# Optimization experiments

Measured on AMD Instinct MI355X. Metric: run time of the kernel, lower is better.

## Reference

```python
import jax, jax.numpy as jnp
import numpy as np

DIM = 128
HEADS = 4
GN_GROUPS = 4
EPS = 1e-5


def setup_inputs() -> dict:
    key = jax.random.key(0)
    ks = jax.random.split(key, 6)
    B, C, H, W = 4, DIM, 64, 64
    x = jax.random.normal(ks[0], (B, C, H, W), dtype=jnp.float32)
    # 1x1 convs are channel matmuls: store as [out_ch, in_ch]
    w_qkv = jax.random.normal(ks[1], (3 * C, C), dtype=jnp.float32) * (C ** -0.5)
    w_out = jax.random.normal(ks[2], (C, C), dtype=jnp.float32) * (C ** -0.5)
    b_out = jax.random.normal(ks[3], (C,), dtype=jnp.float32) * 0.01
    gn_gamma = jnp.ones((C,), dtype=jnp.float32)
    gn_beta = jnp.zeros((C,), dtype=jnp.float32)
    return {"x": x, "w_qkv": w_qkv, "w_out": w_out, "b_out": b_out,
            "gn_gamma": gn_gamma, "gn_beta": gn_beta}


def _attention_block(x, w_qkv, w_out, b_out, gn_gamma, gn_beta):
    b, c, h, w = x.shape
    d = c // HEADS
    scale = d ** -0.5
    # 1x1 conv == per-pixel matmul over channels
    qkv = jnp.einsum('bchw,oc->bohw', x, w_qkv)  # [b, 3c, h, w]
    q, k, v = jnp.split(qkv, 3, axis=1)
    # 'b (h d) x y -> b h (x y) d'
    def to_heads(t):
        return t.reshape(b, HEADS, d, h * w).transpose(0, 1, 3, 2)  # [b, H, N, d]
    q, k, v = to_heads(q), to_heads(k), to_heads(v)
    dots = jnp.einsum('bhnd,bhmd->bhnm', q, k) * scale  # [b, H, N, N]
    attn = jax.nn.softmax(dots, axis=-1)
    out = jnp.einsum('bhnm,bhmd->bhnd', attn, v)  # [b, H, N, d]
    # 'b h (x y) d -> b (h d) x y'
    out = out.transpose(0, 1, 3, 2).reshape(b, c, h, w)
    # output 1x1 conv + bias
    out = jnp.einsum('bchw,oc->bohw', out, w_out) + b_out[None, :, None, None]
    # GroupNorm(4, c)
    g = out.reshape(b, GN_GROUPS, c // GN_GROUPS, h, w)
    mean = g.mean(axis=(2, 3, 4), keepdims=True)
    var = g.var(axis=(2, 3, 4), keepdims=True)
    g = (g - mean) * jax.lax.rsqrt(var + EPS)
    out = g.reshape(b, c, h, w) * gn_gamma[None, :, None, None] + gn_beta[None, :, None, None]
    return out + x


def reference(x, w_qkv, w_out, b_out, gn_gamma, gn_beta):
    return _attention_block(x, w_qkv, w_out, b_out, gn_gamma, gn_beta)
```

## Files before the change

### kernel.cpp

```cpp
#include <hip/hip_runtime.h>

#define DIM   128
#define NPIX  4096
#define DHEAD 32

using u16 = unsigned short;
typedef __attribute__((ext_vector_type(8))) short   short8;
typedef __attribute__((ext_vector_type(8))) u16     ushort8;
typedef __attribute__((ext_vector_type(4))) float   floatx4;
typedef __attribute__((ext_vector_type(2))) unsigned int uint2v;

__device__ __forceinline__ float bf2f(u16 u) {
  union { unsigned int i; float f; } v; v.i = ((unsigned int)u) << 16; return v.f;
}
__device__ __forceinline__ u16 f2bf(float f) {
  union { unsigned int i; float f; } v; v.f = f;
  unsigned int i = v.i;
  return (u16)((i + 0x7FFFu + ((i >> 16) & 1u)) >> 16);
}
__device__ __forceinline__ unsigned int pk2bf(float a, float b) {
  union { float f; unsigned int u; } ua, ub; ua.f = a; ub.f = b;
  return __builtin_amdgcn_perm(ub.u, ua.u, 0x07060302u);
}

template<bool F32> __device__ __forceinline__ float ld1(const void* p, size_t i) {
  if constexpr (F32) return ((const float*)p)[i];
  else               return bf2f(((const u16*)p)[i]);
}
template<bool F32> __device__ __forceinline__ float4 ld4(const void* p, size_t i) {
  if constexpr (F32) {
    return *(const float4*)((const float*)p + i);
  } else {
    const ushort4 u = *(const ushort4*)((const u16*)p + i);
    return make_float4(bf2f(u.x), bf2f(u.y), bf2f(u.z), bf2f(u.w));
  }
}
template<bool F32> __device__ __forceinline__ void st4(void* p, size_t i, float4 v) {
  if constexpr (F32) {
    *(float4*)((float*)p + i) = v;
  } else {
    ushort4 u; u.x = f2bf(v.x); u.y = f2bf(v.y); u.z = f2bf(v.z); u.w = f2bf(v.w);
    *(ushort4*)((u16*)p + i) = u;
  }
}

__global__ void k_detect(const u16* __restrict__ x, int* __restrict__ flag) {
  if (threadIdx.x == 0 && blockIdx.x == 0) {
    int big = 0;
    for (int i = 0; i < 128; ++i) {
      const float v = bf2f(x[i]);
      if (!(fabsf(v) < 1e4f)) big = 1;
    }
    *flag = big;
  }
}

template<bool F32>
__global__ __launch_bounds__(256) void k_qkv(const void* __restrict__ x,
                                             const void* __restrict__ wqkv,
                                             u16* __restrict__ Q,
                                             u16* __restrict__ K,
                                             u16* __restrict__ V,
                                             const int* __restrict__ flag) {
  if (*flag != (F32 ? 1 : 0)) return;
  const int b = blockIdx.z, og = blockIdx.y, pt = blockIdx.x;
  const int tl = threadIdx.x;
  __shared__ float Ws[8][DIM];
  for (int i = tl; i < 8 * DIM; i += 256)
    Ws[i >> 7][i & 127] = ld1<F32>(wqkv, (size_t)(og * 8 + (i >> 7)) * DIM + (i & 127));
  __syncthreads();
  const int p0 = pt * 1024 + tl * 4;
  float acc[8][4];
#pragma unroll
  for (int j = 0; j < 8; ++j) { acc[j][0] = acc[j][1] = acc[j][2] = acc[j][3] = 0.f; }
  const size_t xb = (size_t)b * DIM * NPIX + p0;
  for (int c = 0; c < DIM; ++c) {
    const float4 xv = ld4<F32>(x, xb + (size_t)c * NPIX);
#pragma unroll
    for (int j = 0; j < 8; ++j) {
      const float wv = Ws[j][c];
      acc[j][0] += wv * xv.x; acc[j][1] += wv * xv.y;
      acc[j][2] += wv * xv.z; acc[j][3] += wv * xv.w;
    }
  }
  const int o0 = og * 8;
  if (o0 < 2 * DIM) {
    u16* dst = (o0 < DIM) ? Q : K;
    const int c0 = o0 & 127;
    const int h = c0 >> 5, dd0 = c0 & 31;
    const int bh = b * 4 + h;
#pragma unroll
    for (int t = 0; t < 4; ++t) {
      ushort8 w8;
#pragma unroll
      for (int j = 0; j < 8; ++j) w8[j] = f2bf(acc[j][t]);
      *(ushort8*)(dst + ((size_t)bh * NPIX + p0 + t) * DHEAD + dd0) = w8;
    }
  } else {
#pragma unroll
    for (int j = 0; j < 8; ++j) {
      const int c = (o0 + j) & 127;
      ushort4 w4;
      w4.x = f2bf(acc[j][0]); w4.y = f2bf(acc[j][1]);
      w4.z = f2bf(acc[j][2]); w4.w = f2bf(acc[j][3]);
      *(ushort4*)(V + ((size_t)b * DIM + c) * NPIX + p0) = w4;
    }
  }
}

__global__ __launch_bounds__(256) void k_attn(const u16* __restrict__ Q,
                                              const u16* __restrict__ K,
                                              const u16* __restrict__ V,
                                              u16* __restrict__ O) {
  const int bh = blockIdx.y, qb = blockIdx.x;
  const int tid = threadIdx.x;
  const int wv = tid >> 6, lane = tid & 63;
  const int quad = lane >> 4, l15 = lane & 15;
  const int b = bh >> 2, h = bh & 3;

  __shared__ __align__(16) u16 Klds[64 * 40];
  __shared__ __align__(16) u16 Vlds[32 * 72];
  __shared__ __align__(16) u16 Plds[4 * 16 * 72];
  __shared__ __align__(16) u16 Olds[32 * 72];

  const float SCL = 0.17677669529663687f * 1.4426950408889634f;

  const int qtok = qb * 64 + wv * 16 + l15;
  const short8 qf = *(const short8*)(Q + ((size_t)bh * NPIX + qtok) * DHEAD + quad * 8);

  floatx4 o0 = {0.f, 0.f, 0.f, 0.f}, o1 = {0.f, 0.f, 0.f, 0.f};
  float l_part = 0.f;

  const int skey = tid >> 2, sqt = tid & 3;
  const int sdd = tid >> 3, soc = tid & 7;
  const u16* Kg = K + ((size_t)bh * NPIX + skey) * DHEAD + sqt * 8;
  const u16* Vg = V + ((size_t)(b * DIM + h * DHEAD + sdd)) * NPIX + soc * 8;

  ushort8 kpre = *(const ushort8*)Kg;
  ushort8 vpre = *(const ushort8*)Vg;

  u16* Pw = Plds + wv * 16 * 72;

  for (int ch = 0; ch < 64; ++ch) {
    *(ushort8*)(Klds + skey * 40 + sqt * 8) = kpre;
    *(ushort8*)(Vlds + sdd * 72 + soc * 8) = vpre;
    __syncthreads();
    if (ch + 1 < 64) {
      kpre = *(const ushort8*)(Kg + (size_t)(ch + 1) * 64 * DHEAD);
      vpre = *(const ushort8*)(Vg + (ch + 1) * 64);
    }
#pragma unroll
    for (int sub = 0; sub < 4; ++sub) {
      const short8 af = *(const short8*)(Klds + (sub * 16 + l15) * 40 + quad * 8);
      const floatx4 s = __builtin_amdgcn_mfma_f32_16x16x32_bf16(
          af, qf, (floatx4){0.f, 0.f, 0.f, 0.f}, 0, 0, 0);
      const float p0 = __builtin_amdgcn_exp2f(s[0] * SCL);
      const float p1 = __builtin_amdgcn_exp2f(s[1] * SCL);
      const float p2 = __builtin_amdgcn_exp2f(s[2] * SCL);
      const float p3 = __builtin_amdgcn_exp2f(s[3] * SCL);
      l_part += (p0 + p1) + (p2 + p3);
      uint2v pw;
      pw[0] = pk2bf(p0, p1);
      pw[1] = pk2bf(p2, p3);
      *(uint2v*)(Pw + l15 * 72 + sub * 16 + quad * 4) = pw;
    }
#pragma unroll
    for (int kc = 0; kc < 2; ++kc) {
      const short8 pa  = *(const short8*)(Pw + l15 * 72 + kc * 32 + quad * 8);
      const short8 vb0 = *(const short8*)(Vlds + l15 * 72 + kc * 32 + quad * 8);
      const short8 vb1 = *(const short8*)(Vlds + (16 + l15) * 72 + kc * 32 + quad * 8);
      o0 = __builtin_amdgcn_mfma_f32_16x16x32_bf16(pa, vb0, o0, 0, 0, 0);
      o1 = __builtin_amdgcn_mfma_f32_16x16x32_bf16(pa, vb1, o1, 0, 0, 0);
    }
    __syncthreads();
  }
  float l_run = l_part;
  l_run += __shfl_xor(l_run, 16);
  l_run += __shfl_xor(l_run, 32);
  float linv[4];
#pragma unroll
  for (int r = 0; r < 4; ++r)
    linv[r] = 1.f / __shfl(l_run, (lane & 48) | (quad * 4 + r));
  uint2v w0, w1;
  w0[0] = (unsigned)f2bf(o0[0] * linv[0]) | ((unsigned)f2bf(o0[1] * linv[1]) << 16);
  w0[1] = (unsigned)f2bf(o0[2] * linv[2]) | ((unsigned)f2bf(o0[3] * linv[3]) << 16);
  w1[0] = (unsigned)f2bf(o1[0] * linv[0]) | ((unsigned)f2bf(o1[1] * linv[1]) << 16);
  w1[1] = (unsigned)f2bf(o1[2] * linv[2]) | ((unsigned)f2bf(o1[3] * linv[3]) << 16);
  *(uint2v*)(Olds + l15 * 72 + wv * 16 + quad * 4) = w0;
  *(uint2v*)(Olds + (16 + l15) * 72 + wv * 16 + quad * 4) = w1;
  __syncthreads();
  const int d = tid >> 3, oc = tid & 7;
  const ushort8 ow = *(const ushort8*)(Olds + d * 72 + oc * 8);
  *(ushort8*)(O + ((size_t)(b * DIM + h * DHEAD + d)) * NPIX + qb * 64 + oc * 8) = ow;
}

template<bool F32>
__global__ __launch_bounds__(256) void k_proj(const u16* __restrict__ O,
                                              const void* __restrict__ wout,
                                              const void* __restrict__ bout,
                                              float* __restrict__ Y,
                                              float* __restrict__ Sred,
                                              const int* __restrict__ flag) {
  if (*flag != (F32 ? 1 : 0)) return;
  const int b = blockIdx.z, og = blockIdx.y, pt = blockIdx.x;
  const int tl = threadIdx.x;
  __shared__ float Ws[8][DIM];
  for (int i = tl; i < 8 * DIM; i += 256)
    Ws[i >> 7][i & 127] = ld1<F32>(wout, (size_t)(og * 8 + (i >> 7)) * DIM + (i & 127));
  __syncthreads();
  const int p0 = pt * 1024 + tl * 4;
  float acc[8][4];
#pragma unroll
  for (int j = 0; j < 8; ++j) { acc[j][0] = acc[j][1] = acc[j][2] = acc[j][3] = 0.f; }
  const u16* Ob = O + (size_t)b * DIM * NPIX + p0;
  for (int c = 0; c < DIM; ++c) {
    const ushort4 xv4 = *(const ushort4*)(Ob + (size_t)c * NPIX);
    const float x0 = bf2f(xv4.x), x1 = bf2f(xv4.y), x2 = bf2f(xv4.z), x3 = bf2f(xv4.w);
#pragma unroll
    for (int j = 0; j < 8; ++j) {
      const float wv = Ws[j][c];
      acc[j][0] += wv * x0; acc[j][1] += wv * x1;
      acc[j][2] += wv * x2; acc[j][3] += wv * x3;
    }
  }
  float s1 = 0.f, s2 = 0.f;
#pragma unroll
  for (int j = 0; j < 8; ++j) {
    const int o = og * 8 + j;
    const float bo = ld1<F32>(bout, o);
    float4 y4;
    y4.x = acc[j][0] + bo; y4.y = acc[j][1] + bo;
    y4.z = acc[j][2] + bo; y4.w = acc[j][3] + bo;
    *(float4*)(Y + ((size_t)b * DIM + o) * NPIX + p0) = y4;
    s1 += y4.x + y4.y + y4.z + y4.w;
    s2 += y4.x * y4.x + y4.y * y4.y + y4.z * y4.z + y4.w * y4.w;
  }
  __shared__ float red[2][256];
  red[0][tl] = s1; red[1][tl] = s2;
  __syncthreads();
  for (int off = 128; off >= 1; off >>= 1) {
    if (tl < off) { red[0][tl] += red[0][tl + off]; red[1][tl] += red[1][tl + off]; }
    __syncthreads();
  }
  if (tl == 0) {
    const int g = og >> 2;
    atomicAdd(&Sred[(b * 4 + g) * 2 + 0], red[0][0]);
    atomicAdd(&Sred[(b * 4 + g) * 2 + 1], red[1][0]);
  }
}

template<bool F32>
__global__ __launch_bounds__(256) void k_gn(const float* __restrict__ Y,
                                            const float* __restrict__ Sred,
                                            const void* __restrict__ x,
                                            const void* __restrict__ gamma,
                                            const void* __restrict__ beta,
                                            void* __restrict__ out,
                                            const int* __restrict__ flag) {
  if (*flag != (F32 ? 1 : 0)) return;
  const int idx = (blockIdx.x * 256 + threadIdx.x) * 4;
  const int b = idx >> 19;
  const int c = (idx >> 12) & 127;
  const int g = c >> 5;
  const float inv_n = 1.f / (32.f * 4096.f);
  const float s1 = Sred[(b * 4 + g) * 2 + 0];
  const float s2 = Sred[(b * 4 + g) * 2 + 1];
  const float mean = s1 * inv_n;
  const float var = s2 * inv_n - mean * mean;
  const float rs = rsqrtf(var + 1e-5f);
  const float ga = ld1<F32>(gamma, c) * rs;
  const float be = ld1<F32>(beta, c) - mean * ga;
  const float4 y4 = *(const float4*)(Y + idx);
  const float4 xv = ld4<F32>(x, idx);
  float4 r;
  r.x = y4.x * ga + be + xv.x;
  r.y = y4.y * ga + be + xv.y;
  r.z = y4.z * ga + be + xv.z;
  r.w = y4.w * ga + be + xv.w;
  st4<F32>(out, idx, r);
}

extern "C" void kernel_launch(void* const* d_in, const int* in_sizes, int n_in,
                              void* d_out, int out_size, void* d_ws, size_t ws_size,
                              hipStream_t stream) {
  const void* x     = d_in[0];
  const void* wqkv  = d_in[1];
  const void* wout  = d_in[2];
  const void* bout  = d_in[3];
  const void* gamma = d_in[4];
  const void* beta  = d_in[5];
  char* ws = (char*)d_ws;
  u16*   Q = (u16*)(ws + ((size_t)0  << 20));
  u16*   K = (u16*)(ws + ((size_t)8  << 20));
  u16*   V = (u16*)(ws + ((size_t)16 << 20));
  u16*   O = (u16*)(ws + ((size_t)24 << 20));
  float* Y = (float*)(ws + ((size_t)32 << 20));
  float* S = (float*)(ws + ((size_t)40 << 20));
  int*   F = (int*)(ws + ((size_t)40 << 20) + 128);

  hipMemsetAsync(S, 0, 160, stream);
  k_detect<<<1, 64, 0, stream>>>((const u16*)x, F);

  k_qkv<false><<<dim3(4, 48, 4), 256, 0, stream>>>(x, wqkv, Q, K, V, F);
  k_qkv<true> <<<dim3(4, 48, 4), 256, 0, stream>>>(x, wqkv, Q, K, V, F);
  k_attn<<<dim3(64, 16), 256, 0, stream>>>(Q, K, V, O);
  k_proj<false><<<dim3(4, 16, 4), 256, 0, stream>>>(O, wout, bout, Y, S, F);
  k_proj<true> <<<dim3(4, 16, 4), 256, 0, stream>>>(O, wout, bout, Y, S, F);
  k_gn<false><<<2048, 256, 0, stream>>>(Y, S, x, gamma, beta, d_out, F);
  k_gn<true> <<<2048, 256, 0, stream>>>(Y, S, x, gamma, beta, d_out, F);
}
```

Before: 221.3 us.

## Process 32 queries per wave and double-buffer K/V tiles in attention

Each attention block now covers 128 queries instead of 64, with each wave handling two 16-query tiles. Every K/V tile staged in shared memory is therefore reused across twice as many queries, halving global K/V traffic per query. The K/V shared buffers are also double-buffered, which removes one barrier per chunk. In exchange the grid halves to 512 blocks, which may underfill the GPU's 256 CUs, and register and LDS use per block rise.

New measurement: 214.2 us. 1.03x faster.

```diff
diff --git a/kernel.cpp b/kernel.cpp
--- a/kernel.cpp
+++ b/kernel.cpp
@@ -118,80 +118,111 @@
   const int quad = lane >> 4, l15 = lane & 15;
   const int b = bh >> 2, h = bh & 3;
 
-  __shared__ __align__(16) u16 Klds[64 * 40];
-  __shared__ __align__(16) u16 Vlds[32 * 72];
-  __shared__ __align__(16) u16 Plds[4 * 16 * 72];
-  __shared__ __align__(16) u16 Olds[32 * 72];
+  __shared__ __align__(16) u16 Klds[2][64 * 40];
+  __shared__ __align__(16) u16 Vlds[2][32 * 72];
+  __shared__ __align__(16) u16 Plds[4][32 * 72];
+  __shared__ __align__(16) u16 Olds[32 * 136];
 
   const float SCL = 0.17677669529663687f * 1.4426950408889634f;
 
-  const int qtok = qb * 64 + wv * 16 + l15;
-  const short8 qf = *(const short8*)(Q + ((size_t)bh * NPIX + qtok) * DHEAD + quad * 8);
-
-  floatx4 o0 = {0.f, 0.f, 0.f, 0.f}, o1 = {0.f, 0.f, 0.f, 0.f};
-  float l_part = 0.f;
+  const int qtok0 = qb * 128 + wv * 32 + l15;
+  const short8 qf0 = *(const short8*)(Q + ((size_t)bh * NPIX + qtok0) * DHEAD + quad * 8);
+  const short8 qf1 = *(const short8*)(Q + ((size_t)bh * NPIX + qtok0 + 16) * DHEAD + quad * 8);
+
+  floatx4 o00 = {0.f, 0.f, 0.f, 0.f}, o01 = {0.f, 0.f, 0.f, 0.f};
+  floatx4 o10 = {0.f, 0.f, 0.f, 0.f}, o11 = {0.f, 0.f, 0.f, 0.f};
+  float lp0 = 0.f, lp1 = 0.f;
 
   const int skey = tid >> 2, sqt = tid & 3;
   const int sdd = tid >> 3, soc = tid & 7;
   const u16* Kg = K + ((size_t)bh * NPIX + skey) * DHEAD + sqt * 8;
   const u16* Vg = V + ((size_t)(b * DIM + h * DHEAD + sdd)) * NPIX + soc * 8;
 
-  ushort8 kpre = *(const ushort8*)Kg;
-  ushort8 vpre = *(const ushort8*)Vg;
-
-  u16* Pw = Plds + wv * 16 * 72;
+  {
+    const ushort8 k0 = *(const ushort8*)Kg;
+    const ushort8 v0 = *(const ushort8*)Vg;
+    *(ushort8*)(Klds[0] + skey * 40 + sqt * 8) = k0;
+    *(ushort8*)(Vlds[0] + sdd * 72 + soc * 8) = v0;
+  }
+
+  u16* Pw = Plds[wv];
 
   for (int ch = 0; ch < 64; ++ch) {
-    *(ushort8*)(Klds + skey * 40 + sqt * 8) = kpre;
-    *(ushort8*)(Vlds + sdd * 72 + soc * 8) = vpre;
+    const int cur = ch & 1, nxt = cur ^ 1;
     __syncthreads();
+    ushort8 kpre, vpre;
     if (ch + 1 < 64) {
       kpre = *(const ushort8*)(Kg + (size_t)(ch + 1) * 64 * DHEAD);
       vpre = *(const ushort8*)(Vg + (ch + 1) * 64);
     }
 #pragma unroll
     for (int sub = 0; sub < 4; ++sub) {
-      const short8 af = *(const short8*)(Klds + (sub * 16 + l15) * 40 + quad * 8);
-      const floatx4 s = __builtin_amdgcn_mfma_f32_16x16x32_bf16(
-          af, qf, (floatx4){0.f, 0.f, 0.f, 0.f}, 0, 0, 0);
-      const float p0 = __builtin_amdgcn_exp2f(s[0] * SCL);
-      const float p1 = __builtin_amdgcn_exp2f(s[1] * SCL);
-      const float p2 = __builtin_amdgcn_exp2f(s[2] * SCL);
-      const float p3 = __builtin_amdgcn_exp2f(s[3] * SCL);
-      l_part += (p0 + p1) + (p2 + p3);
-      uint2v pw;
-      pw[0] = pk2bf(p0, p1);
-      pw[1] = pk2bf(p2, p3);
-      *(uint2v*)(Pw + l15 * 72 + sub * 16 + quad * 4) = pw;
+      const short8 af = *(const short8*)(Klds[cur] + (sub * 16 + l15) * 40 + quad * 8);
+      const floatx4 s0 = __builtin_amdgcn_mfma_f32_16x16x32_bf16(
+          af, qf0, (floatx4){0.f, 0.f, 0.f, 0.f}, 0, 0, 0);
+      const floatx4 s1 = __builtin_amdgcn_mfma_f32_16x16x32_bf16(
+          af, qf1, (floatx4){0.f, 0.f, 0.f, 0.f}, 0, 0, 0);
+      const float a0 = __builtin_amdgcn_exp2f(s0[0] * SCL);
+      const float a1 = __builtin_amdgcn_exp2f(s0[1] * SCL);
+      const float a2 = __builtin_amdgcn_exp2f(s0[2] * SCL);
+      const float a3 = __builtin_amdgcn_exp2f(s0[3] * SCL);
+      const float b0 = __builtin_amdgcn_exp2f(s1[0] * SCL);
+      const float b1 = __builtin_amdgcn_exp2f(s1[1] * SCL);
+      const float b2 = __builtin_amdgcn_exp2f(s1[2] * SCL);
+      const float b3 = __builtin_amdgcn_exp2f(s1[3] * SCL);
+      lp0 += (a0 + a1) + (a2 + a3);
+      lp1 += (b0 + b1) + (b2 + b3);
+      uint2v pw0, pw1;
+      pw0[0] = pk2bf(a0, a1); pw0[1] = pk2bf(a2, a3);
+      pw1[0] = pk2bf(b0, b1); pw1[1] = pk2bf(b2, b3);
+      *(uint2v*)(Pw + l15 * 72 + sub * 16 + quad * 4) = pw0;
+      *(uint2v*)(Pw + (16 + l15) * 72 + sub * 16 + quad * 4) = pw1;
     }
 #pragma unroll
     for (int kc = 0; kc < 2; ++kc) {
-      const short8 pa  = *(const short8*)(Pw + l15 * 72 + kc * 32 + quad * 8);
-      const short8 vb0 = *(const short8*)(Vlds + l15 * 72 + kc * 32 + quad * 8);
-      const short8 vb1 = *(const short8*)(Vlds + (16 + l15) * 72 + kc * 32 + quad * 8);
-      o0 = __builtin_amdgcn_mfma_f32_16x16x32_bf16(pa, vb0, o0, 0, 0, 0);
-      o1 = __builtin_amdgcn_mfma_f32_16x16x32_bf16(pa, vb1, o1, 0, 0, 0);
-    }
-    __syncthreads();
-  }
-  float l_run = l_part;
-  l_run += __shfl_xor(l_run, 16);
-  l_run += __shfl_xor(l_run, 32);
-  float linv[4];
-#pragma unroll
-  for (int r = 0; r < 4; ++r)
-    linv[r] = 1.f / __shfl(l_run, (lane & 48) | (quad * 4 + r));
-  uint2v w0, w1;
-  w0[0] = (unsigned)f2bf(o0[0] * linv[0]) | ((unsigned)f2bf(o0[1] * linv[1]) << 16);
-  w0[1] = (unsigned)f2bf(o0[2] * linv[2]) | ((unsigned)f2bf(o0[3] * linv[3]) << 16);
-  w1[0] = (unsigned)f2bf(o1[0] * linv[0]) | ((unsigned)f2bf(o1[1] * linv[1]) << 16);
-  w1[1] = (unsigned)f2bf(o1[2] * linv[2]) | ((unsigned)f2bf(o1[3] * linv[3]) << 16);
-  *(uint2v*)(Olds + l15 * 72 + wv * 16 + quad * 4) = w0;
-  *(uint2v*)(Olds + (16 + l15) * 72 + wv * 16 + quad * 4) = w1;
+      const short8 pa0 = *(const short8*)(Pw + l15 * 72 + kc * 32 + quad * 8);
+      const short8 pa1 = *(const short8*)(Pw + (16 + l15) * 72 + kc * 32 + quad * 8);
+      const short8 vb0 = *(const short8*)(Vlds[cur] + l15 * 72 + kc * 32 + quad * 8);
+      const short8 vb1 = *(const short8*)(Vlds[cur] + (16 + l15) * 72 + kc * 32 + quad * 8);
+      o00 = __builtin_amdgcn_mfma_f32_16x16x32_bf16(pa0, vb0, o00, 0, 0, 0);
+      o01 = __builtin_amdgcn_mfma_f32_16x16x32_bf16(pa0, vb1, o01, 0, 0, 0);
+      o10 = __builtin_amdgcn_mfma_f32_16x16x32_bf16(pa1, vb0, o10, 0, 0, 0);
+      o11 = __builtin_amdgcn_mfma_f32_16x16x32_bf16(pa1, vb1, o11, 0, 0, 0);
+    }
+    if (ch + 1 < 64) {
+      *(ushort8*)(Klds[nxt] + skey * 40 + sqt * 8) = kpre;
+      *(ushort8*)(Vlds[nxt] + sdd * 72 + soc * 8) = vpre;
+    }
+  }
+  float l0 = lp0, l1 = lp1;
+  l0 += __shfl_xor(l0, 16); l0 += __shfl_xor(l0, 32);
+  l1 += __shfl_xor(l1, 16); l1 += __shfl_xor(l1, 32);
+  float li0[4], li1[4];
+#pragma unroll
+  for (int r = 0; r < 4; ++r) {
+    li0[r] = 1.f / __shfl(l0, (lane & 48) | (quad * 4 + r));
+    li1[r] = 1.f / __shfl(l1, (lane & 48) | (quad * 4 + r));
+  }
+  uint2v w00, w01, w10, w11;
+  w00[0] = (unsigned)f2bf(o00[0] * li0[0]) | ((unsigned)f2bf(o00[1] * li0[1]) << 16);
+  w00[1] = (unsigned)f2bf(o00[2] * li0[2]) | ((unsigned)f2bf(o00[3] * li0[3]) << 16);
+  w01[0] = (unsigned)f2bf(o01[0] * li0[0]) | ((unsigned)f2bf(o01[1] * li0[1]) << 16);
+  w01[1] = (unsigned)f2bf(o01[2] * li0[2]) | ((unsigned)f2bf(o01[3] * li0[3]) << 16);
+  w10[0] = (unsigned)f2bf(o10[0] * li1[0]) | ((unsigned)f2bf(o10[1] * li1[1]) << 16);
+  w10[1] = (unsigned)f2bf(o10[2] * li1[2]) | ((unsigned)f2bf(o10[3] * li1[3]) << 16);
+  w11[0] = (unsigned)f2bf(o11[0] * li1[0]) | ((unsigned)f2bf(o11[1] * li1[1]) << 16);
+  w11[1] = (unsigned)f2bf(o11[2] * li1[2]) | ((unsigned)f2bf(o11[3] * li1[3]) << 16);
+  __syncthreads();
+  *(uint2v*)(Olds + l15 * 136 + wv * 32 + quad * 4) = w00;
+  *(uint2v*)(Olds + (16 + l15) * 136 + wv * 32 + quad * 4) = w01;
+  *(uint2v*)(Olds + l15 * 136 + wv * 32 + 16 + quad * 4) = w10;
+  *(uint2v*)(Olds + (16 + l15) * 136 + wv * 32 + 16 + quad * 4) = w11;
   __syncthreads();
   const int d = tid >> 3, oc = tid & 7;
-  const ushort8 ow = *(const ushort8*)(Olds + d * 72 + oc * 8);
-  *(ushort8*)(O + ((size_t)(b * DIM + h * DHEAD + d)) * NPIX + qb * 64 + oc * 8) = ow;
+  const u16* orow = Olds + d * 136;
+  u16* og = O + ((size_t)(b * DIM + h * DHEAD + d)) * NPIX + qb * 128;
+  *(ushort8*)(og + oc * 8)      = *(const ushort8*)(orow + oc * 8);
+  *(ushort8*)(og + 64 + oc * 8) = *(const ushort8*)(orow + 64 + oc * 8);
 }
 
 template<bool F32>
@@ -303,7 +334,7 @@
 
   k_qkv<false><<<dim3(4, 48, 4), 256, 0, stream>>>(x, wqkv, Q, K, V, F);
   k_qkv<true> <<<dim3(4, 48, 4), 256, 0, stream>>>(x, wqkv, Q, K, V, F);
-  k_attn<<<dim3(64, 16), 256, 0, stream>>>(Q, K, V, O);
+  k_attn<<<dim3(32, 16), 256, 0, stream>>>(Q, K, V, O);
   k_proj<false><<<dim3(4, 16, 4), 256, 0, stream>>>(O, wout, bout, Y, S, F);
   k_proj<true> <<<dim3(4, 16, 4), 256, 0, stream>>>(O, wout, bout, Y, S, F);
   k_gn<false><<<2048, 256, 0, stream>>>(Y, S, x, gamma, beta, d_out, F);
```
